# Kernel optimization log

Measured on AMD Instinct MI355X. Metric: run time of the kernel, lower is better.

Reference implementation:

```python
import jax, jax.numpy as jnp
import numpy as np

T_LEN = 1024
N_IN = 512
BATCH = 32
SURR_ALPHA = 4.0  # slope of the sigmoid surrogate gradient


@jax.custom_vjp
def heaviside_sg(x):
    # spike = Heaviside(x); backward uses sigmoid surrogate derivative
    return (x >= 0).astype(x.dtype)

def _hs_fwd(x):
    return heaviside_sg(x), x

def _hs_bwd(x, g):
    s = jax.nn.sigmoid(SURR_ALPHA * x)
    return (g * SURR_ALPHA * s * (1.0 - s),)

heaviside_sg.defvjp(_hs_fwd, _hs_bwd)


def setup_inputs() -> dict:
    key = jax.random.key(0)
    k1, k2, k3 = jax.random.split(key, 3)
    current = jax.random.normal(k1, (T_LEN, BATCH, N_IN), dtype=jnp.float32)
    beta = jax.random.uniform(k2, (N_IN,), dtype=jnp.float32)  # per-channel decay in (0,1)
    v_init = jax.random.normal(k3, (BATCH, N_IN), dtype=jnp.float32)
    v_th = jnp.ones((T_LEN, BATCH, N_IN), dtype=jnp.float32)
    return {"current": current, "beta": beta, "v_init": v_init, "v_th": v_th}


def reference(current, beta, v_init, v_th):
    # Torch version: grouped causal conv1d with kernel beta^{T-1-k}, i.e.
    # membrane[t] = sum_{j<=t} beta^{t-j} * current[j], with current[0] += beta*v_init.
    # Equivalent O(T) linear recurrence: m_t = beta*m_{t-1} + c_t, m_{-1}=v_init.
    def step(m, c):
        m = beta * m + c  # beta (N,) broadcasts over (B,N)
        return m, m

    m_last, membrane = jax.lax.scan(step, v_init, current)  # membrane: (T,B,N)

    # surrogate-gradient spike function
    spikes = heaviside_sg(membrane - v_th)  # (T,B,N)

    # triangular phi kernel: z[t] = sum_{j<=t} (t-j+1)*spikes[j] == double cumsum
    z = jnp.cumsum(jnp.cumsum(spikes, axis=0), axis=0)  # (T,B,N)

    # Block.g: keep entries equal to 1, zero everything else; gradient is identity
    # (the subtracted term is detached in the torch code).
    gz = z - jax.lax.stop_gradient(jnp.where(z == 1.0, 0.0, z))

    return gz, z, m_last  # m_last == membrane[:, :, -1] in torch layout (B,N)
```

## Files before the change

kernel.cpp:

```cpp
#include <hip/hip_runtime.h>


#define T_LEN 1024
#define N_IN  512
#define BN    16384
#define SEG_T 32
#define NSEG  (T_LEN / SEG_T)

__device__ __forceinline__ void gload_lds16(const float* g, float* l) {
    __builtin_amdgcn_global_load_lds(
        (const __attribute__((address_space(1))) void*)g,
        (__attribute__((address_space(3))) void*)l, 16, 0, 0);
}

__device__ __forceinline__ void issue_seg(const float* __restrict__ src,
                                          float* dst, int s, size_t goff) {
#pragma unroll
    for (int j = 0; j < SEG_T / 4; ++j) {
        gload_lds16(src + (size_t)(SEG_T * s + 4 * j) * BN + goff, dst + j * 256);
    }
}

__global__ __launch_bounds__(704, 1) void snn_fused(
        const float* __restrict__ cur, const float* __restrict__ beta,
        const float* __restrict__ vini, const float* __restrict__ vth,
        float* __restrict__ gz, float* __restrict__ zo, float* __restrict__ ml)
{
    __shared__ float ldsC[2][SEG_T * 64];
    __shared__ float ldsV[2][SEG_T * 64];
    __shared__ float zbuf[2][SEG_T][64];

    const int lane   = threadIdx.x & 63;
    const int wave   = threadIdx.x >> 6;
    const int chbase = blockIdx.x * 64;
    const size_t goff = (size_t)chbase + (size_t)(lane >> 4) * BN
                      + (size_t)(4 * (lane & 15));

    float bta = 0.0f, m = 0.0f;
    int C = 0, Z = 0;
    if (wave == 0) {
        bta = beta[(chbase + lane) & (N_IN - 1)];
        m   = vini[chbase + lane];
    }

    const int ww      = wave - 3;
    const int row_sub = lane >> 4;
    const int chgrp   = lane & 15;
    const int myrow   = 4 * ww + row_sub;

    if (wave == 1) issue_seg(cur, &ldsC[0][0], 0, goff);
    if (wave == 2) issue_seg(vth, &ldsV[0][0], 0, goff);
    __syncthreads();

    for (int s = 0; s <= NSEG; ++s) {
        if (wave == 1 && s + 1 < NSEG) issue_seg(cur, &ldsC[(s + 1) & 1][0], s + 1, goff);
        if (wave == 2 && s + 1 < NSEG) issue_seg(vth, &ldsV[(s + 1) & 1][0], s + 1, goff);

        if (wave == 0 && s < NSEG) {
            const int cb = s & 1;
            const float* lc = &ldsC[cb][lane];
            const float* lv = &ldsV[cb][lane];
            float cc[SEG_T], vv[SEG_T];
#pragma unroll
            for (int t = 0; t < SEG_T; ++t) {
                cc[t] = lc[t * 64];
                vv[t] = lv[t * 64];
            }
#pragma unroll
            for (int t = 0; t < SEG_T; ++t) {
                m = fmaf(bta, m, cc[t]);
                const int sp = (m >= vv[t]) ? 1 : 0;
                C += sp;
                Z += C;
                zbuf[cb][t][lane] = (float)Z;
            }
            if (s == NSEG - 1) ml[chbase + lane] = m;
        }

        if (wave >= 3 && s >= 1) {
            const int ds_ = s - 1;
            const int pb = ds_ & 1;
            const float4 zq = *reinterpret_cast<const float4*>(
                                  &zbuf[pb][myrow][4 * chgrp]);
            const float4 gf = make_float4(zq.x == 1.0f ? 1.0f : 0.0f,
                                          zq.y == 1.0f ? 1.0f : 0.0f,
                                          zq.z == 1.0f ? 1.0f : 0.0f,
                                          zq.w == 1.0f ? 1.0f : 0.0f);
            const size_t off = (size_t)(ds_ * 32 + myrow) * BN
                             + chbase + 4 * chgrp;
            *reinterpret_cast<float4*>(gz + off) = gf;
            *reinterpret_cast<float4*>(zo + off) = zq;
        }

        if (s < NSEG) __syncthreads();
    }
}

extern "C" void kernel_launch(void* const* d_in, const int* in_sizes, int n_in,
                              void* d_out, int out_size, void* d_ws, size_t ws_size,
                              hipStream_t stream) {
    const float* cur  = (const float*)d_in[0];
    const float* beta = (const float*)d_in[1];
    const float* vini = (const float*)d_in[2];
    const float* vth  = (const float*)d_in[3];
    float* gz = (float*)d_out;
    float* zo = gz + (size_t)T_LEN * BN;
    float* ml = zo + (size_t)T_LEN * BN;

    snn_fused<<<BN / 64, 704, 0, stream>>>(cur, beta, vini, vth, gz, zo, ml);
}
```

Measured before the change: 241.1 us.

## Deepen global-to-LDS prefetch pipeline to four segments with partial vmcnt waits

Grows the LDS staging ring for current and threshold from two to four segments, so loads for three segments ahead are in flight at once. The full __syncthreads is replaced with a raw s_barrier, preceded by selective s_waitcnt vmcnt(16/8/0) so loader waves wait only on the oldest segment. The aim is to hide global memory latency behind the serial recurrence on wave 0. It uses more LDS and depends on hand-tuned waitcnt counts, so wrong counts could cause races.

```diff
diff --git a/kernel.cpp b/kernel.cpp
--- a/kernel.cpp
+++ b/kernel.cpp
@@ -6,6 +6,7 @@
 #define BN    16384
 #define SEG_T 32
 #define NSEG  (T_LEN / SEG_T)
+#define DEPTH 4
 
 __device__ __forceinline__ void gload_lds16(const float* g, float* l) {
     __builtin_amdgcn_global_load_lds(
@@ -26,8 +27,8 @@
         const float* __restrict__ vini, const float* __restrict__ vth,
         float* __restrict__ gz, float* __restrict__ zo, float* __restrict__ ml)
 {
-    __shared__ float ldsC[2][SEG_T * 64];
-    __shared__ float ldsV[2][SEG_T * 64];
+    __shared__ float ldsC[DEPTH][SEG_T * 64];
+    __shared__ float ldsV[DEPTH][SEG_T * 64];
     __shared__ float zbuf[2][SEG_T][64];
 
     const int lane   = threadIdx.x & 63;
@@ -48,16 +49,29 @@
     const int chgrp   = lane & 15;
     const int myrow   = 4 * ww + row_sub;
 
-    if (wave == 1) issue_seg(cur, &ldsC[0][0], 0, goff);
-    if (wave == 2) issue_seg(vth, &ldsV[0][0], 0, goff);
-    __syncthreads();
+    if (wave == 1) {
+        issue_seg(cur, &ldsC[0][0], 0, goff);
+        issue_seg(cur, &ldsC[1][0], 1, goff);
+        issue_seg(cur, &ldsC[2][0], 2, goff);
+    }
+    if (wave == 2) {
+        issue_seg(vth, &ldsV[0][0], 0, goff);
+        issue_seg(vth, &ldsV[1][0], 1, goff);
+        issue_seg(vth, &ldsV[2][0], 2, goff);
+    }
+    if (wave == 1 || wave == 2)
+        asm volatile("s_waitcnt vmcnt(16)" ::: "memory");
+    __builtin_amdgcn_s_barrier();
 
     for (int s = 0; s <= NSEG; ++s) {
-        if (wave == 1 && s + 1 < NSEG) issue_seg(cur, &ldsC[(s + 1) & 1][0], s + 1, goff);
-        if (wave == 2 && s + 1 < NSEG) issue_seg(vth, &ldsV[(s + 1) & 1][0], s + 1, goff);
+        if (s + DEPTH - 1 < NSEG) {
+            const int nb = (s + DEPTH - 1) & (DEPTH - 1);
+            if (wave == 1) issue_seg(cur, &ldsC[nb][0], s + DEPTH - 1, goff);
+            if (wave == 2) issue_seg(vth, &ldsV[nb][0], s + DEPTH - 1, goff);
+        }
 
         if (wave == 0 && s < NSEG) {
-            const int cb = s & 1;
+            const int cb = s & (DEPTH - 1);
             const float* lc = &ldsC[cb][lane];
             const float* lv = &ldsV[cb][lane];
             float cc[SEG_T], vv[SEG_T];
@@ -72,16 +86,15 @@
                 const int sp = (m >= vv[t]) ? 1 : 0;
                 C += sp;
                 Z += C;
-                zbuf[cb][t][lane] = (float)Z;
+                zbuf[s & 1][t][lane] = (float)Z;
             }
             if (s == NSEG - 1) ml[chbase + lane] = m;
         }
 
         if (wave >= 3 && s >= 1) {
             const int ds_ = s - 1;
-            const int pb = ds_ & 1;
             const float4 zq = *reinterpret_cast<const float4*>(
-                                  &zbuf[pb][myrow][4 * chgrp]);
+                                  &zbuf[ds_ & 1][myrow][4 * chgrp]);
             const float4 gf = make_float4(zq.x == 1.0f ? 1.0f : 0.0f,
                                           zq.y == 1.0f ? 1.0f : 0.0f,
                                           zq.z == 1.0f ? 1.0f : 0.0f,
@@ -92,7 +105,19 @@
             *reinterpret_cast<float4*>(zo + off) = zq;
         }
 
-        if (s < NSEG) __syncthreads();
+        if (s < NSEG) {
+            if (wave == 1 || wave == 2) {
+                if (s <= NSEG - 4)
+                    asm volatile("s_waitcnt vmcnt(16)" ::: "memory");
+                else if (s == NSEG - 3)
+                    asm volatile("s_waitcnt vmcnt(8)" ::: "memory");
+                else
+                    asm volatile("s_waitcnt vmcnt(0)" ::: "memory");
+            }
+            if (wave == 0)
+                asm volatile("s_waitcnt lgkmcnt(0)" ::: "memory");
+            __builtin_amdgcn_s_barrier();
+        }
     }
 }
 
```

New measurement: 242.0 us. No clear change (+0.4%).

## Prefetch recurrence inputs into registers and drop LDS staging waves

Applied to the files above, without the earlier changes.

The compute wave now loads current and threshold directly from global memory into double-buffered register arrays, prefetching the next segment while scanning the current one. This removes the two loader waves and the LDS staging buffers. Synchronisation switches from __syncthreads to raw s_barrier calls with explicit waitcnts, which cuts the block from 704 to 576 threads. Per-lane scalar global loads (4-byte, strided by BN) replace 16-byte global-to-LDS loads, which may lower memory efficiency and raise register pressure.

```diff
diff --git a/kernel.cpp b/kernel.cpp
--- a/kernel.cpp
+++ b/kernel.cpp
@@ -7,92 +7,90 @@
 #define SEG_T 32
 #define NSEG  (T_LEN / SEG_T)
 
-__device__ __forceinline__ void gload_lds16(const float* g, float* l) {
-    __builtin_amdgcn_global_load_lds(
-        (const __attribute__((address_space(1))) void*)g,
-        (__attribute__((address_space(3))) void*)l, 16, 0, 0);
-}
-
-__device__ __forceinline__ void issue_seg(const float* __restrict__ src,
-                                          float* dst, int s, size_t goff) {
-#pragma unroll
-    for (int j = 0; j < SEG_T / 4; ++j) {
-        gload_lds16(src + (size_t)(SEG_T * s + 4 * j) * BN + goff, dst + j * 256);
-    }
-}
-
-__global__ __launch_bounds__(704, 1) void snn_fused(
+__global__ __launch_bounds__(576, 1) void snn_fused(
         const float* __restrict__ cur, const float* __restrict__ beta,
         const float* __restrict__ vini, const float* __restrict__ vth,
         float* __restrict__ gz, float* __restrict__ zo, float* __restrict__ ml)
 {
-    __shared__ float ldsC[2][SEG_T * 64];
-    __shared__ float ldsV[2][SEG_T * 64];
     __shared__ float zbuf[2][SEG_T][64];
 
     const int lane   = threadIdx.x & 63;
     const int wave   = threadIdx.x >> 6;
     const int chbase = blockIdx.x * 64;
-    const size_t goff = (size_t)chbase + (size_t)(lane >> 4) * BN
-                      + (size_t)(4 * (lane & 15));
 
-    float bta = 0.0f, m = 0.0f;
-    int C = 0, Z = 0;
     if (wave == 0) {
-        bta = beta[(chbase + lane) & (N_IN - 1)];
-        m   = vini[chbase + lane];
-    }
+        const int i = chbase + lane;
+        const float bta = beta[i & (N_IN - 1)];
+        float m = vini[i];
+        int C = 0, Z = 0;
+        const float* __restrict__ cp = cur + i;
+        const float* __restrict__ vp = vth + i;
 
-    const int ww      = wave - 3;
-    const int row_sub = lane >> 4;
-    const int chgrp   = lane & 15;
-    const int myrow   = 4 * ww + row_sub;
+        float cA[SEG_T], vA[SEG_T], cB[SEG_T], vB[SEG_T];
 
-    if (wave == 1) issue_seg(cur, &ldsC[0][0], 0, goff);
-    if (wave == 2) issue_seg(vth, &ldsV[0][0], 0, goff);
-    __syncthreads();
+#pragma unroll
+        for (int t = 0; t < SEG_T; ++t) {
+            cA[t] = cp[(size_t)t * BN];
+            vA[t] = vp[(size_t)t * BN];
+        }
 
-    for (int s = 0; s <= NSEG; ++s) {
-        if (wave == 1 && s + 1 < NSEG) issue_seg(cur, &ldsC[(s + 1) & 1][0], s + 1, goff);
-        if (wave == 2 && s + 1 < NSEG) issue_seg(vth, &ldsV[(s + 1) & 1][0], s + 1, goff);
-
-        if (wave == 0 && s < NSEG) {
-            const int cb = s & 1;
-            const float* lc = &ldsC[cb][lane];
-            const float* lv = &ldsV[cb][lane];
-            float cc[SEG_T], vv[SEG_T];
+        auto step = [&](float (&Xc)[SEG_T], float (&Xv)[SEG_T],
+                        float (&Yc)[SEG_T], float (&Yv)[SEG_T],
+                        int segNext, float* zb) {
+            asm volatile("s_waitcnt vmcnt(0)" ::: "memory");
+            if (segNext < NSEG) {
+                const float* __restrict__ c2 = cp + (size_t)segNext * SEG_T * BN;
+                const float* __restrict__ v2 = vp + (size_t)segNext * SEG_T * BN;
+#pragma unroll
+                for (int t = 0; t < SEG_T; ++t) {
+                    Yc[t] = c2[(size_t)t * BN];
+                    Yv[t] = v2[(size_t)t * BN];
+                }
+            }
+            __builtin_amdgcn_sched_barrier(0);
 #pragma unroll
             for (int t = 0; t < SEG_T; ++t) {
-                cc[t] = lc[t * 64];
-                vv[t] = lv[t * 64];
-            }
-#pragma unroll
-            for (int t = 0; t < SEG_T; ++t) {
-                m = fmaf(bta, m, cc[t]);
-                const int sp = (m >= vv[t]) ? 1 : 0;
+                m = fmaf(bta, m, Xc[t]);
+                const int sp = (m >= Xv[t]) ? 1 : 0;
                 C += sp;
                 Z += C;
-                zbuf[cb][t][lane] = (float)Z;
+                zb[t * 64] = (float)Z;
             }
-            if (s == NSEG - 1) ml[chbase + lane] = m;
+            asm volatile("s_waitcnt lgkmcnt(0)" ::: "memory");
+        };
+
+        step(cA, vA, cB, vB, 1, &zbuf[0][0][lane]);
+        __builtin_amdgcn_s_barrier();
+#pragma unroll 1
+        for (int k = 0; k < (NSEG - 2) / 2; ++k) {
+            step(cB, vB, cA, vA, 2 * k + 2, &zbuf[1][0][lane]);
+            __builtin_amdgcn_s_barrier();
+            step(cA, vA, cB, vB, 2 * k + 3, &zbuf[0][0][lane]);
+            __builtin_amdgcn_s_barrier();
         }
+        step(cB, vB, cA, vA, NSEG, &zbuf[1][0][lane]);
+        ml[i] = m;
+        __builtin_amdgcn_s_barrier();
+    } else {
+        const int ww      = wave - 1;
+        const int row_sub = lane >> 4;
+        const int chgrp   = lane & 15;
+        const int myrow   = 4 * ww + row_sub;
 
-        if (wave >= 3 && s >= 1) {
-            const int ds_ = s - 1;
-            const int pb = ds_ & 1;
+#pragma unroll 1
+        for (int n = 0; n < NSEG; ++n) {
+            __builtin_amdgcn_s_barrier();
             const float4 zq = *reinterpret_cast<const float4*>(
-                                  &zbuf[pb][myrow][4 * chgrp]);
+                                  &zbuf[n & 1][myrow][4 * chgrp]);
             const float4 gf = make_float4(zq.x == 1.0f ? 1.0f : 0.0f,
                                           zq.y == 1.0f ? 1.0f : 0.0f,
                                           zq.z == 1.0f ? 1.0f : 0.0f,
                                           zq.w == 1.0f ? 1.0f : 0.0f);
-            const size_t off = (size_t)(ds_ * 32 + myrow) * BN
+            const size_t off = (size_t)(n * 32 + myrow) * BN
                              + chbase + 4 * chgrp;
             *reinterpret_cast<float4*>(gz + off) = gf;
             *reinterpret_cast<float4*>(zo + off) = zq;
         }
-
-        if (s < NSEG) __syncthreads();
     }
 }
 
@@ -107,5 +105,5 @@
     float* zo = gz + (size_t)T_LEN * BN;
     float* ml = zo + (size_t)T_LEN * BN;
 
-    snn_fused<<<BN / 64, 704, 0, stream>>>(cur, beta, vini, vth, gz, zo, ml);
+    snn_fused<<<BN / 64, 576, 0, stream>>>(cur, beta, vini, vth, gz, zo, ml);
 }
```

Result: no change. 239.3 us (-0.7%).
